# Kernel tuning notes

Measured on AMD Instinct MI355X. Metric: run time of the kernel, lower is better.

Reference implementation:

```python
import jax, jax.numpy as jnp
import numpy as np

N = 1048576
INPUT_CH = 3
INPUT_CH_VIEWS = 3
HIDDEN = 64
GEO_FEAT = 15


def setup_inputs() -> dict:
    key = jax.random.key(0)
    ks = jax.random.split(key, 8)
    def w(k, out_d, in_d):
        # torch nn.Linear default init: U(-1/sqrt(in), 1/sqrt(in)), weight shape [out, in]
        bound = 1.0 / np.sqrt(in_d)
        return jax.random.uniform(k, (out_d, in_d), jnp.float32, -bound, bound)
    return {
        "x": jax.random.normal(ks[0], (N, INPUT_CH + INPUT_CH_VIEWS), jnp.float32),
        "sw0": w(ks[1], HIDDEN, INPUT_CH),
        "sw1": w(ks[2], HIDDEN, HIDDEN),
        "sw2": w(ks[3], 1 + GEO_FEAT, HIDDEN),
        "cw0": w(ks[4], HIDDEN, INPUT_CH_VIEWS + GEO_FEAT),
        "cw1": w(ks[5], HIDDEN, HIDDEN),
        "cw2": w(ks[6], HIDDEN, HIDDEN),
        "cw3": w(ks[7], 3, HIDDEN),
    }


def reference(x, sw0, sw1, sw2, cw0, cw1, cw2, cw3):
    input_pts = x[..., :INPUT_CH]          # [N, 3]
    input_views = x[..., INPUT_CH:]        # [N, 3]

    # sigma network: Linear(no bias) + ReLU (no ReLU on last layer)
    h = jax.nn.relu(input_pts @ sw0.T)     # [N, 64]
    h = jax.nn.relu(h @ sw1.T)             # [N, 64]
    h = h @ sw2.T                          # [N, 16]
    sigma = h[..., 0]                      # [N]
    geo_feat = h[..., 1:]                  # [N, 15]

    # color network
    h = jnp.concatenate([input_views, geo_feat], axis=-1)  # [N, 18]
    h = jax.nn.relu(h @ cw0.T)             # [N, 64]
    h = jax.nn.relu(h @ cw1.T)             # [N, 64]
    h = jax.nn.relu(h @ cw2.T)             # [N, 64]
    color = h @ cw3.T                      # [N, 3]

    return jnp.concatenate([color, sigma[..., None]], axis=-1)  # [N, 4]
```

## Files before the change

### kernel.cpp

```cpp
#include <hip/hip_runtime.h>
#include <stdint.h>

typedef __attribute__((ext_vector_type(8))) _Float16 half8;
typedef __attribute__((ext_vector_type(2))) __fp16 fp16x2;
typedef __attribute__((ext_vector_type(16))) float floatx16;
typedef __attribute__((ext_vector_type(2))) short s16x2;
typedef unsigned int u32;
typedef unsigned short u16;

#define TPW 4

__device__ __forceinline__ u32 pkf16(float a, float b) {
  union { fp16x2 v; u32 u; } c;
  c.v = __builtin_amdgcn_cvt_pkrtz(a, b);
  return c.u;
}

__device__ __forceinline__ u32 relu_pk(u32 t) {
  union { u32 u; s16x2 v; } c;
  c.u = t;
  s16x2 zz = {0, 0};
  c.v = __builtin_elementwise_max(c.v, zz);
  return c.u;
}

__device__ __forceinline__ u16 rtnh(float a) {
  union { _Float16 h; u16 u; } c;
  c.h = (_Float16)a;
  return c.u;
}

__device__ __forceinline__ int sigperm(int k) {
  int r = k & 15;
  int s = (r & 3) | ((r & 4) << 1) | ((r & 8) >> 1);
  return (k & ~15) | s;
}

__device__ __forceinline__ half8 packhalf(const floatx16 a, int base, bool relu) {
  union { u32 u[4]; half8 v; } r;
#pragma unroll
  for (int i = 0; i < 4; ++i) {
    u32 t = pkf16(a[base + 2 * i], a[base + 2 * i + 1]);
    r.u[i] = relu ? relu_pk(t) : t;
  }
  return r.v;
}

#define MFMA(A, B, C) __builtin_amdgcn_mfma_f32_32x32x16_f16(A, B, C, 0, 0, 0)

#define NFRAG 38

__global__ void build_pool(
    const float* __restrict__ w_s0, const float* __restrict__ w_s1,
    const float* __restrict__ w_s2, const float* __restrict__ w_c0,
    const float* __restrict__ w_c1, const float* __restrict__ w_c2,
    const float* __restrict__ w_c3, uint4* __restrict__ pool) {
  const int f = blockIdx.x;
  const int lane = threadIdx.x;
  const int m = lane & 31;
  const int kb = (lane >> 5) << 3;

  union { u16 e[8]; uint4 q; } u;
  if (f < 2) {
    const int row = f * 32 + m;
#pragma unroll
    for (int j = 0; j < 8; ++j) {
      const int k = kb + j;
      u.e[j] = (k < 3) ? rtnh(w_s0[row * 3 + k]) : (u16)0;
    }
  } else if (f < 10) {
    const int g = f - 2, rt = g >> 2, ks = g & 3;
    const int row = rt * 32 + m;
#pragma unroll
    for (int j = 0; j < 8; ++j)
      u.e[j] = rtnh(w_s1[row * 64 + sigperm(ks * 16 + kb + j)]);
  } else if (f < 14) {
    const int ks = f - 10;
    const int row = (m < 16) ? m : 0;
#pragma unroll
    for (int j = 0; j < 8; ++j) {
      u16 v = rtnh(w_s2[row * 64 + sigperm(ks * 16 + kb + j)]);
      u.e[j] = (m < 16) ? v : (u16)0;
    }
  } else if (f < 18) {
    const int g = f - 14, rt = g >> 1, ks = g & 1;
    const int row = rt * 32 + m;
#pragma unroll
    for (int j = 0; j < 8; ++j) {
      if (ks == 0) {
        const int c = sigperm(kb + j);
        u16 v = rtnh(w_c0[row * 18 + (c + 2)]);
        u.e[j] = (c == 0) ? (u16)0 : v;
      } else {
        const int kk = kb + j;
        u16 v = rtnh(w_c0[row * 18 + kk]);
        u.e[j] = (kk < 3) ? v : (u16)0;
      }
    }
  } else if (f < 26) {
    const int g = f - 18, rt = g >> 2, ks = g & 3;
    const int row = rt * 32 + m;
#pragma unroll
    for (int j = 0; j < 8; ++j)
      u.e[j] = rtnh(w_c1[row * 64 + sigperm(ks * 16 + kb + j)]);
  } else if (f < 34) {
    const int g = f - 26, rt = g >> 2, ks = g & 3;
    const int row = rt * 32 + m;
#pragma unroll
    for (int j = 0; j < 8; ++j)
      u.e[j] = rtnh(w_c2[row * 64 + sigperm(ks * 16 + kb + j)]);
  } else {
    const int ks = f - 34;
    const int row = (m < 3) ? m : 0;
#pragma unroll
    for (int j = 0; j < 8; ++j) {
      u16 v = rtnh(w_c3[row * 64 + sigperm(ks * 16 + kb + j)]);
      u.e[j] = (m < 3) ? v : (u16)0;
    }
  }
  pool[f * 64 + lane] = u.q;
}

__global__ __launch_bounds__(256, 3) void nerf_fused(
    const float* __restrict__ x, const uint4* __restrict__ pool,
    float* __restrict__ out, int npts) {
  __shared__ __align__(16) u16 wl[NFRAG * 512];

  {
    uint4* lp = (uint4*)wl;
    for (int i = threadIdx.x; i < NFRAG * 64; i += 256) lp[i] = pool[i];
  }
  __syncthreads();

  const int lane = threadIdx.x & 63;
  const int wid = threadIdx.x >> 6;
  const int m = lane & 31;
  const int hi = lane >> 5;

#define LD(F) (*(const half8*)(wl + (F) * 512 + lane * 8))

  const int ntiles = npts >> 5;
  const int wgid = blockIdx.x * 4 + wid;
  const floatx16 z = (floatx16)0.0f;

  for (int t = 0; t < TPW; t += 2) {
    const int tileA = wgid * TPW + t;
    if (tileA >= ntiles) break;
    const int ptA = (tileA << 5) | m;
    const int ptB = ptA + 32;

    const float2* xpA = (const float2*)(x + (size_t)ptA * 6);
    const float2 a0 = xpA[0], a1 = xpA[1], a2 = xpA[2];
    const float2* xpB = (const float2*)(x + (size_t)ptB * 6);
    const float2 c0_ = xpB[0], c1_ = xpB[1], c2_ = xpB[2];

    union { u32 u[4]; half8 v; } bxA, bvA, bxB, bvB;
    bxA.u[0] = hi ? 0u : pkf16(a0.x, a0.y);
    bxA.u[1] = hi ? 0u : pkf16(a1.x, 0.0f);
    bxA.u[2] = 0u; bxA.u[3] = 0u;
    bvA.u[0] = hi ? 0u : pkf16(a1.y, a2.x);
    bvA.u[1] = hi ? 0u : pkf16(a2.y, 0.0f);
    bvA.u[2] = 0u; bvA.u[3] = 0u;
    bxB.u[0] = hi ? 0u : pkf16(c0_.x, c0_.y);
    bxB.u[1] = hi ? 0u : pkf16(c1_.x, 0.0f);
    bxB.u[2] = 0u; bxB.u[3] = 0u;
    bvB.u[0] = hi ? 0u : pkf16(c1_.y, c2_.x);
    bvB.u[1] = hi ? 0u : pkf16(c2_.y, 0.0f);
    bvB.u[2] = 0u; bvB.u[3] = 0u;

    floatx16 hA0, hA1, hB0, hB1;
    half8 w;

    w = LD(0); hA0 = MFMA(w, bxA.v, z); hB0 = MFMA(w, bxB.v, z);
    w = LD(1); hA1 = MFMA(w, bxA.v, z); hB1 = MFMA(w, bxB.v, z);
    half8 bA0 = packhalf(hA0, 0, true), bA1 = packhalf(hA0, 8, true);
    half8 bA2 = packhalf(hA1, 0, true), bA3 = packhalf(hA1, 8, true);
    half8 bB0 = packhalf(hB0, 0, true), bB1 = packhalf(hB0, 8, true);
    half8 bB2 = packhalf(hB1, 0, true), bB3 = packhalf(hB1, 8, true);

    w = LD(2); hA0 = MFMA(w, bA0, z);   hB0 = MFMA(w, bB0, z);
    w = LD(6); hA1 = MFMA(w, bA0, z);   hB1 = MFMA(w, bB0, z);
    w = LD(3); hA0 = MFMA(w, bA1, hA0); hB0 = MFMA(w, bB1, hB0);
    w = LD(7); hA1 = MFMA(w, bA1, hA1); hB1 = MFMA(w, bB1, hB1);
    w = LD(4); hA0 = MFMA(w, bA2, hA0); hB0 = MFMA(w, bB2, hB0);
    w = LD(8); hA1 = MFMA(w, bA2, hA1); hB1 = MFMA(w, bB2, hB1);
    w = LD(5); hA0 = MFMA(w, bA3, hA0); hB0 = MFMA(w, bB3, hB0);
    w = LD(9); hA1 = MFMA(w, bA3, hA1); hB1 = MFMA(w, bB3, hB1);
    bA0 = packhalf(hA0, 0, true); bA1 = packhalf(hA0, 8, true);
    bA2 = packhalf(hA1, 0, true); bA3 = packhalf(hA1, 8, true);
    bB0 = packhalf(hB0, 0, true); bB1 = packhalf(hB0, 8, true);
    bB2 = packhalf(hB1, 0, true); bB3 = packhalf(hB1, 8, true);

    floatx16 hsA, hsB;
    w = LD(10); hsA = MFMA(w, bA0, z);   hsB = MFMA(w, bB0, z);
    w = LD(11); hsA = MFMA(w, bA1, hsA); hsB = MFMA(w, bB1, hsB);
    w = LD(12); hsA = MFMA(w, bA2, hsA); hsB = MFMA(w, bB2, hsB);
    w = LD(13); hsA = MFMA(w, bA3, hsA); hsB = MFMA(w, bB3, hsB);
    const float sigmaA = hsA[0], sigmaB = hsB[0];
    const half8 bs2A = packhalf(hsA, 0, false);
    const half8 bs2B = packhalf(hsB, 0, false);

    w = LD(14); hA0 = MFMA(w, bs2A, z);    hB0 = MFMA(w, bs2B, z);
    w = LD(16); hA1 = MFMA(w, bs2A, z);    hB1 = MFMA(w, bs2B, z);
    w = LD(15); hA0 = MFMA(w, bvA.v, hA0); hB0 = MFMA(w, bvB.v, hB0);
    w = LD(17); hA1 = MFMA(w, bvA.v, hA1); hB1 = MFMA(w, bvB.v, hB1);
    bA0 = packhalf(hA0, 0, true); bA1 = packhalf(hA0, 8, true);
    bA2 = packhalf(hA1, 0, true); bA3 = packhalf(hA1, 8, true);
    bB0 = packhalf(hB0, 0, true); bB1 = packhalf(hB0, 8, true);
    bB2 = packhalf(hB1, 0, true); bB3 = packhalf(hB1, 8, true);

    w = LD(18); hA0 = MFMA(w, bA0, z);   hB0 = MFMA(w, bB0, z);
    w = LD(22); hA1 = MFMA(w, bA0, z);   hB1 = MFMA(w, bB0, z);
    w = LD(19); hA0 = MFMA(w, bA1, hA0); hB0 = MFMA(w, bB1, hB0);
    w = LD(23); hA1 = MFMA(w, bA1, hA1); hB1 = MFMA(w, bB1, hB1);
    w = LD(20); hA0 = MFMA(w, bA2, hA0); hB0 = MFMA(w, bB2, hB0);
    w = LD(24); hA1 = MFMA(w, bA2, hA1); hB1 = MFMA(w, bB2, hB1);
    w = LD(21); hA0 = MFMA(w, bA3, hA0); hB0 = MFMA(w, bB3, hB0);
    w = LD(25); hA1 = MFMA(w, bA3, hA1); hB1 = MFMA(w, bB3, hB1);
    bA0 = packhalf(hA0, 0, true); bA1 = packhalf(hA0, 8, true);
    bA2 = packhalf(hA1, 0, true); bA3 = packhalf(hA1, 8, true);
    bB0 = packhalf(hB0, 0, true); bB1 = packhalf(hB0, 8, true);
    bB2 = packhalf(hB1, 0, true); bB3 = packhalf(hB1, 8, true);

    w = LD(26); hA0 = MFMA(w, bA0, z);   hB0 = MFMA(w, bB0, z);
    w = LD(30); hA1 = MFMA(w, bA0, z);   hB1 = MFMA(w, bB0, z);
    w = LD(27); hA0 = MFMA(w, bA1, hA0); hB0 = MFMA(w, bB1, hB0);
    w = LD(31); hA1 = MFMA(w, bA1, hA1); hB1 = MFMA(w, bB1, hB1);
    w = LD(28); hA0 = MFMA(w, bA2, hA0); hB0 = MFMA(w, bB2, hB0);
    w = LD(32); hA1 = MFMA(w, bA2, hA1); hB1 = MFMA(w, bB2, hB1);
    w = LD(29); hA0 = MFMA(w, bA3, hA0); hB0 = MFMA(w, bB3, hB0);
    w = LD(33); hA1 = MFMA(w, bA3, hA1); hB1 = MFMA(w, bB3, hB1);
    bA0 = packhalf(hA0, 0, true); bA1 = packhalf(hA0, 8, true);
    bA2 = packhalf(hA1, 0, true); bA3 = packhalf(hA1, 8, true);
    bB0 = packhalf(hB0, 0, true); bB1 = packhalf(hB0, 8, true);
    bB2 = packhalf(hB1, 0, true); bB3 = packhalf(hB1, 8, true);

    floatx16 hcA, hcB;
    w = LD(34); hcA = MFMA(w, bA0, z);   hcB = MFMA(w, bB0, z);
    w = LD(35); hcA = MFMA(w, bA1, hcA); hcB = MFMA(w, bB1, hcB);
    w = LD(36); hcA = MFMA(w, bA2, hcA); hcB = MFMA(w, bB2, hcB);
    w = LD(37); hcA = MFMA(w, bA3, hcA); hcB = MFMA(w, bB3, hcB);

    if (lane < 32) {
      float4 oA, oB;
      oA.x = hcA[0]; oA.y = hcA[1]; oA.z = hcA[2]; oA.w = sigmaA;
      oB.x = hcB[0]; oB.y = hcB[1]; oB.z = hcB[2]; oB.w = sigmaB;
      *(float4*)(out + (size_t)ptA * 4) = oA;
      *(float4*)(out + (size_t)ptB * 4) = oB;
    }
  }
#undef LD
}

extern "C" void kernel_launch(void* const* d_in, const int* in_sizes, int n_in,
                              void* d_out, int out_size, void* d_ws, size_t ws_size,
                              hipStream_t stream) {
  const float* x = (const float*)d_in[0];
  const float* sw0 = (const float*)d_in[1];
  const float* sw1 = (const float*)d_in[2];
  const float* sw2 = (const float*)d_in[3];
  const float* cw0 = (const float*)d_in[4];
  const float* cw1 = (const float*)d_in[5];
  const float* cw2 = (const float*)d_in[6];
  const float* cw3 = (const float*)d_in[7];
  float* out = (float*)d_out;
  uint4* pool = (uint4*)d_ws;

  const int npts = in_sizes[0] / 6;
  const int ntiles = npts >> 5;
  const int blocks = (ntiles + 4 * TPW - 1) / (4 * TPW);

  build_pool<<<NFRAG, 64, 0, stream>>>(sw0, sw1, sw2, cw0, cw1, cw2, cw3, pool);
  nerf_fused<<<blocks, 256, 0, stream>>>(x, pool, out, npts);
}
```

Baseline: 112.4 us.

## Fold sigma output layer into color layer 0 and compute sigma via fdot2

Folds the linear geo-feature layer (sw2 rows 1..15) into the first color layer by precomputing the product cw0[:,3:] @ sw2[1:] in the weight-prep kernel. The color layer then reads the 64-wide hidden activations directly, and sigma is computed separately with packed fp16 dot products plus a cross-half shuffle. This removes the dedicated sigma/geo MFMA layer and one pack step, but adds four K-steps to the color layer's first matmul and some VALU dot work. It also raises the LDS weight pool and register footprint, which is why the launch bound drops from 3 to 2 blocks per CU. The fused weight is rounded to fp16 once after accumulation in fp32, so numerics differ slightly from the original path.

```diff
diff --git a/kernel.cpp b/kernel.cpp
--- a/kernel.cpp
+++ b/kernel.cpp
@@ -30,6 +30,12 @@
   return c.u;
 }
 
+__device__ __forceinline__ fp16x2 as_h2(u32 x) {
+  union { u32 u; fp16x2 h; } c;
+  c.u = x;
+  return c.h;
+}
+
 __device__ __forceinline__ int sigperm(int k) {
   int r = k & 15;
   int s = (r & 3) | ((r & 4) << 1) | ((r & 8) >> 1);
@@ -48,7 +54,7 @@
 
 #define MFMA(A, B, C) __builtin_amdgcn_mfma_f32_32x32x16_f16(A, B, C, 0, 0, 0)
 
-#define NFRAG 38
+#define NFRAG 44
 
 __global__ void build_pool(
     const float* __restrict__ w_s0, const float* __restrict__ w_s1,
@@ -58,7 +64,8 @@
   const int f = blockIdx.x;
   const int lane = threadIdx.x;
   const int m = lane & 31;
-  const int kb = (lane >> 5) << 3;
+  const int hi = lane >> 5;
+  const int kb = hi << 3;
 
   union { u16 e[8]; uint4 q; } u;
   if (f < 2) {
@@ -74,54 +81,58 @@
 #pragma unroll
     for (int j = 0; j < 8; ++j)
       u.e[j] = rtnh(w_s1[row * 64 + sigperm(ks * 16 + kb + j)]);
-  } else if (f < 14) {
-    const int ks = f - 10;
-    const int row = (m < 16) ? m : 0;
-#pragma unroll
-    for (int j = 0; j < 8; ++j) {
-      u16 v = rtnh(w_s2[row * 64 + sigperm(ks * 16 + kb + j)]);
-      u.e[j] = (m < 16) ? v : (u16)0;
-    }
   } else if (f < 18) {
-    const int g = f - 14, rt = g >> 1, ks = g & 1;
-    const int row = rt * 32 + m;
-#pragma unroll
-    for (int j = 0; j < 8; ++j) {
-      if (ks == 0) {
-        const int c = sigperm(kb + j);
-        u16 v = rtnh(w_c0[row * 18 + (c + 2)]);
-        u.e[j] = (c == 0) ? (u16)0 : v;
-      } else {
-        const int kk = kb + j;
-        u16 v = rtnh(w_c0[row * 18 + kk]);
-        u.e[j] = (kk < 3) ? v : (u16)0;
-      }
-    }
-  } else if (f < 26) {
-    const int g = f - 18, rt = g >> 2, ks = g & 3;
+    const int g = f - 10, rt = g >> 2, ks = g & 3;
+    const int row = rt * 32 + m;
+#pragma unroll
+    for (int j = 0; j < 8; ++j) {
+      const int col = sigperm(ks * 16 + kb + j);
+      float acc = 0.f;
+      for (int g2 = 0; g2 < 15; ++g2)
+        acc += w_c0[row * 18 + 3 + g2] * w_s2[(1 + g2) * 64 + col];
+      u.e[j] = rtnh(acc);
+    }
+  } else if (f < 20) {
+    const int rt = f - 18;
+    const int row = rt * 32 + m;
+#pragma unroll
+    for (int j = 0; j < 8; ++j) {
+      const int kk = kb + j;
+      u16 v = rtnh(w_c0[row * 18 + ((kk < 3) ? kk : 0)]);
+      u.e[j] = (kk < 3) ? v : (u16)0;
+    }
+  } else if (f < 28) {
+    const int g = f - 20, rt = g >> 2, ks = g & 3;
     const int row = rt * 32 + m;
 #pragma unroll
     for (int j = 0; j < 8; ++j)
       u.e[j] = rtnh(w_c1[row * 64 + sigperm(ks * 16 + kb + j)]);
-  } else if (f < 34) {
-    const int g = f - 26, rt = g >> 2, ks = g & 3;
+  } else if (f < 36) {
+    const int g = f - 28, rt = g >> 2, ks = g & 3;
     const int row = rt * 32 + m;
 #pragma unroll
     for (int j = 0; j < 8; ++j)
       u.e[j] = rtnh(w_c2[row * 64 + sigperm(ks * 16 + kb + j)]);
-  } else {
-    const int ks = f - 34;
+  } else if (f < 40) {
+    const int ks = f - 36;
     const int row = (m < 3) ? m : 0;
 #pragma unroll
     for (int j = 0; j < 8; ++j) {
       u16 v = rtnh(w_c3[row * 64 + sigperm(ks * 16 + kb + j)]);
       u.e[j] = (m < 3) ? v : (u16)0;
     }
+  } else {
+    const int q = f - 40;
+#pragma unroll
+    for (int j = 0; j < 8; ++j) {
+      const int c = 16 * q + (j & 3) + 8 * (j >> 2) + 4 * hi;
+      u.e[j] = rtnh(w_s2[c]);
+    }
   }
   pool[f * 64 + lane] = u.q;
 }
 
-__global__ __launch_bounds__(256, 3) void nerf_fused(
+__global__ __launch_bounds__(256, 2) void nerf_fused(
     const float* __restrict__ x, const uint4* __restrict__ pool,
     float* __restrict__ out, int npts) {
   __shared__ __align__(16) u16 wl[NFRAG * 512];
@@ -138,6 +149,14 @@
   const int hi = lane >> 5;
 
 #define LD(F) (*(const half8*)(wl + (F) * 512 + lane * 8))
+
+  u32 wsig[16];
+#pragma unroll
+  for (int q = 0; q < 4; ++q) {
+    const u32* p = (const u32*)(wl + (40 + q) * 512 + lane * 8);
+#pragma unroll
+    for (int i = 0; i < 4; ++i) wsig[q * 4 + i] = p[i];
+  }
 
   const int ntiles = npts >> 5;
   const int wgid = blockIdx.x * 4 + wid;
@@ -191,60 +210,72 @@
     bB0 = packhalf(hB0, 0, true); bB1 = packhalf(hB0, 8, true);
     bB2 = packhalf(hB1, 0, true); bB3 = packhalf(hB1, 8, true);
 
-    floatx16 hsA, hsB;
-    w = LD(10); hsA = MFMA(w, bA0, z);   hsB = MFMA(w, bB0, z);
-    w = LD(11); hsA = MFMA(w, bA1, hsA); hsB = MFMA(w, bB1, hsB);
-    w = LD(12); hsA = MFMA(w, bA2, hsA); hsB = MFMA(w, bB2, hsB);
-    w = LD(13); hsA = MFMA(w, bA3, hsA); hsB = MFMA(w, bB3, hsB);
-    const float sigmaA = hsA[0], sigmaB = hsB[0];
-    const half8 bs2A = packhalf(hsA, 0, false);
-    const half8 bs2B = packhalf(hsB, 0, false);
-
-    w = LD(14); hA0 = MFMA(w, bs2A, z);    hB0 = MFMA(w, bs2B, z);
-    w = LD(16); hA1 = MFMA(w, bs2A, z);    hB1 = MFMA(w, bs2B, z);
-    w = LD(15); hA0 = MFMA(w, bvA.v, hA0); hB0 = MFMA(w, bvB.v, hB0);
-    w = LD(17); hA1 = MFMA(w, bvA.v, hA1); hB1 = MFMA(w, bvB.v, hB1);
+    float sA = 0.f, sB = 0.f;
+    {
+      union { half8 v; u32 u[4]; } fA[4] = {{bA0}, {bA1}, {bA2}, {bA3}};
+      union { half8 v; u32 u[4]; } fB[4] = {{bB0}, {bB1}, {bB2}, {bB3}};
+#pragma unroll
+      for (int q = 0; q < 4; ++q)
+#pragma unroll
+        for (int i = 0; i < 4; ++i) {
+          sA = __builtin_amdgcn_fdot2(as_h2(fA[q].u[i]), as_h2(wsig[q * 4 + i]), sA, false);
+          sB = __builtin_amdgcn_fdot2(as_h2(fB[q].u[i]), as_h2(wsig[q * 4 + i]), sB, false);
+        }
+    }
+    sA += __shfl_xor(sA, 32, 64);
+    sB += __shfl_xor(sB, 32, 64);
+
+    w = LD(18); hA0 = MFMA(w, bvA.v, z); hB0 = MFMA(w, bvB.v, z);
+    w = LD(19); hA1 = MFMA(w, bvA.v, z); hB1 = MFMA(w, bvB.v, z);
+    w = LD(10); hA0 = MFMA(w, bA0, hA0); hB0 = MFMA(w, bB0, hB0);
+    w = LD(14); hA1 = MFMA(w, bA0, hA1); hB1 = MFMA(w, bB0, hB1);
+    w = LD(11); hA0 = MFMA(w, bA1, hA0); hB0 = MFMA(w, bB1, hB0);
+    w = LD(15); hA1 = MFMA(w, bA1, hA1); hB1 = MFMA(w, bB1, hB1);
+    w = LD(12); hA0 = MFMA(w, bA2, hA0); hB0 = MFMA(w, bB2, hB0);
+    w = LD(16); hA1 = MFMA(w, bA2, hA1); hB1 = MFMA(w, bB2, hB1);
+    w = LD(13); hA0 = MFMA(w, bA3, hA0); hB0 = MFMA(w, bB3, hB0);
+    w = LD(17); hA1 = MFMA(w, bA3, hA1); hB1 = MFMA(w, bB3, hB1);
     bA0 = packhalf(hA0, 0, true); bA1 = packhalf(hA0, 8, true);
     bA2 = packhalf(hA1, 0, true); bA3 = packhalf(hA1, 8, true);
     bB0 = packhalf(hB0, 0, true); bB1 = packhalf(hB0, 8, true);
     bB2 = packhalf(hB1, 0, true); bB3 = packhalf(hB1, 8, true);
 
-    w = LD(18); hA0 = MFMA(w, bA0, z);   hB0 = MFMA(w, bB0, z);
-    w = LD(22); hA1 = MFMA(w, bA0, z);   hB1 = MFMA(w, bB0, z);
-    w = LD(19); hA0 = MFMA(w, bA1, hA0); hB0 = MFMA(w, bB1, hB0);
-    w = LD(23); hA1 = MFMA(w, bA1, hA1); hB1 = MFMA(w, bB1, hB1);
-    w = LD(20); hA0 = MFMA(w, bA2, hA0); hB0 = MFMA(w, bB2, hB0);
-    w = LD(24); hA1 = MFMA(w, bA2, hA1); hB1 = MFMA(w, bB2, hB1);
-    w = LD(21); hA0 = MFMA(w, bA3, hA0); hB0 = MFMA(w, bB3, hB0);
-    w = LD(25); hA1 = MFMA(w, bA3, hA1); hB1 = MFMA(w, bB3, hB1);
+    w = LD(20); hA0 = MFMA(w, bA0, z);   hB0 = MFMA(w, bB0, z);
+    w = LD(24); hA1 = MFMA(w, bA0, z);   hB1 = MFMA(w, bB0, z);
+    w = LD(21); hA0 = MFMA(w, bA1, hA0); hB0 = MFMA(w, bB1, hB0);
+    w = LD(25); hA1 = MFMA(w, bA1, hA1); hB1 = MFMA(w, bB1, hB1);
+    w = LD(22); hA0 = MFMA(w, bA2, hA0); hB0 = MFMA(w, bB2, hB0);
+    w = LD(26); hA1 = MFMA(w, bA2, hA1); hB1 = MFMA(w, bB2, hB1);
+    w = LD(23); hA0 = MFMA(w, bA3, hA0); hB0 = MFMA(w, bB3, hB0);
+    w = LD(27); hA1 = MFMA(w, bA3, hA1); hB1 = MFMA(w, bB3, hB1);
     bA0 = packhalf(hA0, 0, true); bA1 = packhalf(hA0, 8, true);
     bA2 = packhalf(hA1, 0, true); bA3 = packhalf(hA1, 8, true);
     bB0 = packhalf(hB0, 0, true); bB1 = packhalf(hB0, 8, true);
     bB2 = packhalf(hB1, 0, true); bB3 = packhalf(hB1, 8, true);
 
-    w = LD(26); hA0 = MFMA(w, bA0, z);   hB0 = MFMA(w, bB0, z);
-    w = LD(30); hA1 = MFMA(w, bA0, z);   hB1 = MFMA(w, bB0, z);
-    w = LD(27); hA0 = MFMA(w, bA1, hA0); hB0 = MFMA(w, bB1, hB0);
-    w = LD(31); hA1 = MFMA(w, bA1, hA1); hB1 = MFMA(w, bB1, hB1);
-    w = LD(28); hA0 = MFMA(w, bA2, hA0); hB0 = MFMA(w, bB2, hB0);
-    w = LD(32); hA1 = MFMA(w, bA2, hA1); hB1 = MFMA(w, bB2, hB1);
-    w = LD(29); hA0 = MFMA(w, bA3, hA0); hB0 = MFMA(w, bB3, hB0);
-    w = LD(33); hA1 = MFMA(w, bA3, hA1); hB1 = MFMA(w, bB3, hB1);
+    w = LD(28); hA0 = MFMA(w, bA0, z);   hB0 = MFMA(w, bB0, z);
+    w = LD(32); hA1 = MFMA(w, bA0, z);   hB1 = MFMA(w, bB0, z);
+    w = LD(29); hA0 = MFMA(w, bA1, hA0); hB0 = MFMA(w, bB1, hB0);
+    w = LD(33); hA1 = MFMA(w, bA1, hA1); hB1 = MFMA(w, bB1, hB1);
+    w = LD(30); hA0 = MFMA(w, bA2, hA0); hB0 = MFMA(w, bB2, hB0);
+    w = LD(34); hA1 = MFMA(w, bA2, hA1); hB1 = MFMA(w, bB2, hB1);
+    w = LD(31); hA0 = MFMA(w, bA3, hA0); hB0 = MFMA(w, bB3, hB0);
+    w = LD(35); hA1 = MFMA(w, bA3, hA1); hB1 = MFMA(w, bB3, hB1);
     bA0 = packhalf(hA0, 0, true); bA1 = packhalf(hA0, 8, true);
     bA2 = packhalf(hA1, 0, true); bA3 = packhalf(hA1, 8, true);
     bB0 = packhalf(hB0, 0, true); bB1 = packhalf(hB0, 8, true);
     bB2 = packhalf(hB1, 0, true); bB3 = packhalf(hB1, 8, true);
 
     floatx16 hcA, hcB;
-    w = LD(34); hcA = MFMA(w, bA0, z);   hcB = MFMA(w, bB0, z);
-    w = LD(35); hcA = MFMA(w, bA1, hcA); hcB = MFMA(w, bB1, hcB);
-    w = LD(36); hcA = MFMA(w, bA2, hcA); hcB = MFMA(w, bB2, hcB);
-    w = LD(37); hcA = MFMA(w, bA3, hcA); hcB = MFMA(w, bB3, hcB);
+    w = LD(36); hcA = MFMA(w, bA0, z);   hcB = MFMA(w, bB0, z);
+    w = LD(37); hcA = MFMA(w, bA1, hcA); hcB = MFMA(w, bB1, hcB);
+    w = LD(38); hcA = MFMA(w, bA2, hcA); hcB = MFMA(w, bB2, hcB);
+    w = LD(39); hcA = MFMA(w, bA3, hcA); hcB = MFMA(w, bB3, hcB);
 
     if (lane < 32) {
       float4 oA, oB;
-      oA.x = hcA[0]; oA.y = hcA[1]; oA.z = hcA[2]; oA.w = sigmaA;
-      oB.x = hcB[0]; oB.y = hcB[1]; oB.z = hcB[2]; oB.w = sigmaB;
+      oA.x = hcA[0]; oA.y = hcA[1]; oA.z = hcA[2]; oA.w = sA;
+      oB.x = hcB[0]; oB.y = hcB[1]; oB.z = hcB[2]; oB.w = sB;
       *(float4*)(out + (size_t)ptA * 4) = oA;
       *(float4*)(out + (size_t)ptB * 4) = oB;
     }
```

Result: slower. 116.4 us (+3.5%).
